# Performance work log

Measured on AMD Instinct MI355X. Metric: run time of the kernel, lower is better.

The kernel has to match this reference:

```python
import jax, jax.numpy as jnp
import numpy as np

N_EXPERTS = 8
EMB = 1024
HID = 2816


def setup_inputs() -> dict:
    key = jax.random.key(0)
    k1, k2, k3, k4, k5 = jax.random.split(key, 5)
    x = jax.random.normal(k1, (2, 2048, EMB), dtype=jnp.float32)
    w_router = jax.random.normal(k2, (EMB, N_EXPERTS), dtype=jnp.float32) * 0.02
    w1 = jax.random.normal(k3, (N_EXPERTS, EMB, HID), dtype=jnp.float32) * 0.02
    w3 = jax.random.normal(k4, (N_EXPERTS, EMB, HID), dtype=jnp.float32) * 0.02
    w2 = jax.random.normal(k5, (N_EXPERTS, HID, EMB), dtype=jnp.float32) * 0.02
    return {"x": x, "w_router": w_router, "w1": w1, "w3": w3, "w2": w2,
            "n_experts_per_token": 2}


def reference(x, w_router, w1, w3, w2, n_experts_per_token):
    # x: (b, s, d) -> flatten to tokens (t, d)
    orig_shape = x.shape
    xf = x.reshape(-1, orig_shape[-1])                      # (t, d)
    scores = xf @ w_router                                  # (t, E)
    top_v, top_i = jax.lax.top_k(scores, n_experts_per_token)  # (t, k)
    top_p = jax.nn.softmax(top_v, axis=-1)                  # (t, k)
    # dense per-token gate over experts (top-k indices are distinct)
    gates = jnp.sum(jax.nn.one_hot(top_i, w_router.shape[-1], dtype=x.dtype)
                    * top_p[..., None], axis=1)             # (t, E)
    # SwiGLU for every expert (dense reference for the masked dispatch)
    h = jnp.einsum('td,edh->teh', xf, w1)                   # (t, E, H)
    g = jnp.einsum('td,edh->teh', xf, w3)                   # (t, E, H)
    expert_out = jnp.einsum('teh,ehd->ted', jax.nn.silu(h) * g, w2)  # (t, E, d)
    y = jnp.einsum('ted,te->td', expert_out, gates)
    return y.reshape(orig_shape)
```

## Files before the change

### kernel.cpp

```cpp
#include <hip/hip_runtime.h>
#include <hip/hip_bf16.h>

#define N_EXPERTS 8
#define EMB 1024
#define HID 2816
#define NTOK 4096
#define NSLOT (NTOK * 2)
#define TLIST NTOK

typedef float f32x4 __attribute__((ext_vector_type(4)));
typedef short short8 __attribute__((ext_vector_type(8)));

static __device__ __forceinline__ unsigned short f2bf(float v) {
    __hip_bfloat16 b = __float2bfloat16(v);
    return *reinterpret_cast<unsigned short*>(&b);
}

static __device__ __forceinline__ void ldst16(const unsigned short* g, unsigned short* l) {
    __builtin_amdgcn_global_load_lds(
        (const __attribute__((address_space(1))) unsigned int*)g,
        (__attribute__((address_space(3))) unsigned int*)l,
        16, 0, 0);
}

__global__ __launch_bounds__(256) void transpose_cvt(const float* __restrict__ in,
                                                     unsigned short* __restrict__ out,
                                                     int R, int C) {
    __shared__ unsigned short tile[64][68];
    int e = blockIdx.z;
    int r0 = blockIdx.y * 64, c0 = blockIdx.x * 64;
    const float* src = in + (size_t)e * R * C;
    unsigned short* dst = out + (size_t)e * R * C;
    int tid = threadIdx.x;
#pragma unroll
    for (int i = 0; i < 4; ++i) {
        int lin = i * 256 + tid;
        int r = lin >> 4, c4 = (lin & 15) * 4;
        float4 v = *(const float4*)&src[(size_t)(r0 + r) * C + c0 + c4];
        ushort4 b;
        b.x = f2bf(v.x); b.y = f2bf(v.y); b.z = f2bf(v.z); b.w = f2bf(v.w);
        *(ushort4*)&tile[r][c4] = b;
    }
    __syncthreads();
#pragma unroll
    for (int i = 0; i < 4; ++i) {
        int lin = i * 256 + tid;
        int c = lin >> 4, r4 = (lin & 15) * 4;
        ushort4 b;
        b.x = tile[r4 + 0][c]; b.y = tile[r4 + 1][c];
        b.z = tile[r4 + 2][c]; b.w = tile[r4 + 3][c];
        *(ushort4*)&dst[(size_t)(c0 + c) * R + r0 + r4] = b;
    }
}

__global__ __launch_bounds__(64) void router_kernel(const float* __restrict__ x,
                                                    const float* __restrict__ wr,
                                                    unsigned short* __restrict__ xbf,
                                                    int* __restrict__ sel,
                                                    float* __restrict__ gates) {
    int t = blockIdx.x, lane = threadIdx.x;
    const float* xr = x + (size_t)t * EMB;
    float acc[N_EXPERTS];
#pragma unroll
    for (int e = 0; e < N_EXPERTS; ++e) acc[e] = 0.f;
    for (int d = lane; d < EMB; d += 64) {
        float xv = xr[d];
        xbf[(size_t)t * EMB + d] = f2bf(xv);
        const float* w = wr + d * N_EXPERTS;
#pragma unroll
        for (int e = 0; e < N_EXPERTS; ++e) acc[e] += xv * w[e];
    }
#pragma unroll
    for (int off = 32; off; off >>= 1) {
#pragma unroll
        for (int e = 0; e < N_EXPERTS; ++e) acc[e] += __shfl_xor(acc[e], off, 64);
    }
    if (lane == 0) {
        int b0 = 0; float v0 = acc[0];
#pragma unroll
        for (int e = 1; e < N_EXPERTS; ++e) if (acc[e] > v0) { v0 = acc[e]; b0 = e; }
        int b1 = -1; float v1 = -1e30f;
#pragma unroll
        for (int e = 0; e < N_EXPERTS; ++e) if (e != b0 && acc[e] > v1) { v1 = acc[e]; b1 = e; }
        float g0 = 1.f / (1.f + expf(v1 - v0));
        float g1 = 1.f - g0;
        sel[t] = b0 | (b1 << 8);
        gates[2 * t] = g0;
        gates[2 * t + 1] = g1;
    }
}

__global__ __launch_bounds__(256) void build_lists(const int* __restrict__ sel,
                                                   int* __restrict__ counts,
                                                   int* __restrict__ lists) {
    int e = blockIdx.x;
    int tid = threadIdx.x, lane = tid & 63, wid = tid >> 6;
    __shared__ int wsum[4];
    __shared__ int running;
    if (tid == 0) running = 0;
    __syncthreads();
    for (int base = 0; base < NTOK; base += 256) {
        int tok = base + tid;
        int s = sel[tok];
        int e0 = s & 0xff, e1 = (s >> 8) & 0xff;
        bool take = (e0 == e) || (e1 == e);
        int slot = (e0 == e) ? 2 * tok : 2 * tok + 1;
        unsigned long long b = __ballot(take);
        int lp = __popcll(b & ((1ull << lane) - 1ull));
        if (lane == 0) wsum[wid] = __popcll(b);
        __syncthreads();
        int off = running;
        for (int w = 0; w < wid; ++w) off += wsum[w];
        if (take) lists[e * TLIST + off + lp] = slot;
        __syncthreads();
        if (tid == 0) running += wsum[0] + wsum[1] + wsum[2] + wsum[3];
        __syncthreads();
    }
    if (tid == 0) counts[e] = running;
}

__global__ __launch_bounds__(256) void gemm1_kernel(const unsigned short* __restrict__ xbf,
                                                    const unsigned short* __restrict__ w1T,
                                                    const unsigned short* __restrict__ w3T,
                                                    unsigned short* __restrict__ h,
                                                    const int* __restrict__ counts,
                                                    const int* __restrict__ lists) {
    int e = blockIdx.z;
    int cnt = counts[e];
    int rt = blockIdx.y;
    if (rt * 128 >= cnt) return;
    int n0 = blockIdx.x * 64;

    __shared__ unsigned short As[128 * 32];
    __shared__ unsigned short B1s[64 * 32];
    __shared__ unsigned short B3s[64 * 32];
    __shared__ int slotArr[128];

    int tid = threadIdx.x;
    if (tid < 128) {
        int r = rt * 128 + tid;
        slotArr[tid] = (r < cnt) ? lists[e * TLIST + r] : -1;
    }
    __syncthreads();

    int lane = tid & 63, wid = tid >> 6;
    int seg = lane >> 2, chunk = lane & 3;

    int rA0 = wid * 32 + seg, rA1 = wid * 32 + 16 + seg;
    int s0 = slotArr[rA0], s1 = slotArr[rA1];
    int t0 = s0 >= 0 ? (s0 >> 1) : 0, t1 = s1 >= 0 ? (s1 >> 1) : 0;
    const unsigned short* gA0 = xbf + (size_t)t0 * EMB + chunk * 8;
    const unsigned short* gA1 = xbf + (size_t)t1 * EMB + chunk * 8;
    int rB = n0 + wid * 16 + seg;
    const unsigned short* gB1 = w1T + ((size_t)e * HID + rB) * EMB + chunk * 8;
    const unsigned short* gB3 = w3T + ((size_t)e * HID + rB) * EMB + chunk * 8;
    unsigned short* lA0 = &As[wid * 1024];
    unsigned short* lA1 = &As[wid * 1024 + 512];
    unsigned short* lB1 = &B1s[wid * 512];
    unsigned short* lB3 = &B3s[wid * 512];

    int wr = wid >> 1, wc = wid & 1;
    int lrow = lane & 15, quad = lane >> 4;

    f32x4 zero4 = {0.f, 0.f, 0.f, 0.f};
    f32x4 acc1[4][2], acc3[4][2];
#pragma unroll
    for (int mt = 0; mt < 4; ++mt)
#pragma unroll
        for (int nt = 0; nt < 2; ++nt) { acc1[mt][nt] = zero4; acc3[mt][nt] = zero4; }

    const int KT = EMB / 32;
    for (int kt = 0; kt < KT; ++kt) {
        ldst16(gA0, lA0); ldst16(gA1, lA1);
        ldst16(gB1, lB1); ldst16(gB3, lB3);
        gA0 += 32; gA1 += 32; gB1 += 32; gB3 += 32;
        __builtin_amdgcn_s_waitcnt(0);
        __syncthreads();
        short8 af[4], b1f[2], b3f[2];
#pragma unroll
        for (int mt = 0; mt < 4; ++mt)
            af[mt] = *(const short8*)&As[(wr * 64 + mt * 16 + lrow) * 32 + quad * 8];
#pragma unroll
        for (int nt = 0; nt < 2; ++nt) {
            b1f[nt] = *(const short8*)&B1s[(wc * 32 + nt * 16 + lrow) * 32 + quad * 8];
            b3f[nt] = *(const short8*)&B3s[(wc * 32 + nt * 16 + lrow) * 32 + quad * 8];
        }
#pragma unroll
        for (int mt = 0; mt < 4; ++mt)
#pragma unroll
            for (int nt = 0; nt < 2; ++nt) {
                acc1[mt][nt] = __builtin_amdgcn_mfma_f32_16x16x32_bf16(af[mt], b1f[nt], acc1[mt][nt], 0, 0, 0);
                acc3[mt][nt] = __builtin_amdgcn_mfma_f32_16x16x32_bf16(af[mt], b3f[nt], acc3[mt][nt], 0, 0, 0);
            }
        __syncthreads();
    }

#pragma unroll
    for (int mt = 0; mt < 4; ++mt) {
#pragma unroll
        for (int i = 0; i < 4; ++i) {
            int r = wr * 64 + mt * 16 + quad * 4 + i;
            int slot = slotArr[r];
            if (slot < 0) continue;
#pragma unroll
            for (int nt = 0; nt < 2; ++nt) {
                float v1 = acc1[mt][nt][i];
                float v3 = acc3[mt][nt][i];
                float hv = v1 / (1.f + __expf(-v1)) * v3;
                int c = n0 + wc * 32 + nt * 16 + lrow;
                h[(size_t)slot * HID + c] = f2bf(hv);
            }
        }
    }
}

__global__ __launch_bounds__(256) void gemm2_kernel(const unsigned short* __restrict__ h,
                                                    const unsigned short* __restrict__ w2T,
                                                    float* __restrict__ oslot,
                                                    const int* __restrict__ counts,
                                                    const int* __restrict__ lists,
                                                    const float* __restrict__ gates) {
    int e = blockIdx.z;
    int cnt = counts[e];
    int rt = blockIdx.y;
    if (rt * 128 >= cnt) return;
    int n0 = blockIdx.x * 128;

    __shared__ unsigned short As[128 * 32];
    __shared__ unsigned short Bs[128 * 32];
    __shared__ int slotArr[128];

    int tid = threadIdx.x;
    if (tid < 128) {
        int r = rt * 128 + tid;
        slotArr[tid] = (r < cnt) ? lists[e * TLIST + r] : -1;
    }
    __syncthreads();

    int lane = tid & 63, wid = tid >> 6;
    int seg = lane >> 2, chunk = lane & 3;

    int rA0 = wid * 32 + seg, rA1 = wid * 32 + 16 + seg;
    int s0 = slotArr[rA0], s1 = slotArr[rA1];
    const unsigned short* gA0 = h + (size_t)(s0 < 0 ? 0 : s0) * HID + chunk * 8;
    const unsigned short* gA1 = h + (size_t)(s1 < 0 ? 0 : s1) * HID + chunk * 8;
    int rB0 = n0 + wid * 32 + seg, rB1 = rB0 + 16;
    const unsigned short* gB0 = w2T + ((size_t)e * EMB + rB0) * HID + chunk * 8;
    const unsigned short* gB1 = w2T + ((size_t)e * EMB + rB1) * HID + chunk * 8;
    unsigned short* lA0 = &As[wid * 1024];
    unsigned short* lA1 = &As[wid * 1024 + 512];
    unsigned short* lB0 = &Bs[wid * 1024];
    unsigned short* lB1 = &Bs[wid * 1024 + 512];

    int wr = wid >> 1, wc = wid & 1;
    int lrow = lane & 15, quad = lane >> 4;

    f32x4 zero4 = {0.f, 0.f, 0.f, 0.f};
    f32x4 acc[4][4];
#pragma unroll
    for (int mt = 0; mt < 4; ++mt)
#pragma unroll
        for (int nt = 0; nt < 4; ++nt) acc[mt][nt] = zero4;

    const int KT = HID / 32;
    for (int kt = 0; kt < KT; ++kt) {
        ldst16(gA0, lA0); ldst16(gA1, lA1);
        ldst16(gB0, lB0); ldst16(gB1, lB1);
        gA0 += 32; gA1 += 32; gB0 += 32; gB1 += 32;
        __builtin_amdgcn_s_waitcnt(0);
        __syncthreads();
        short8 af[4], bf[4];
#pragma unroll
        for (int mt = 0; mt < 4; ++mt)
            af[mt] = *(const short8*)&As[(wr * 64 + mt * 16 + lrow) * 32 + quad * 8];
#pragma unroll
        for (int nt = 0; nt < 4; ++nt)
            bf[nt] = *(const short8*)&Bs[(wc * 64 + nt * 16 + lrow) * 32 + quad * 8];
#pragma unroll
        for (int mt = 0; mt < 4; ++mt)
#pragma unroll
            for (int nt = 0; nt < 4; ++nt)
                acc[mt][nt] = __builtin_amdgcn_mfma_f32_16x16x32_bf16(af[mt], bf[nt], acc[mt][nt], 0, 0, 0);
        __syncthreads();
    }

#pragma unroll
    for (int mt = 0; mt < 4; ++mt) {
#pragma unroll
        for (int i = 0; i < 4; ++i) {
            int r = wr * 64 + mt * 16 + quad * 4 + i;
            int slot = slotArr[r];
            if (slot < 0) continue;
            float g = gates[slot];
#pragma unroll
            for (int nt = 0; nt < 4; ++nt) {
                int c = n0 + wc * 64 + nt * 16 + lrow;
                oslot[(size_t)slot * EMB + c] = g * acc[mt][nt][i];
            }
        }
    }
}

__global__ __launch_bounds__(256) void combine_kernel(const float* __restrict__ oslot,
                                                      float* __restrict__ out) {
    int gid = blockIdx.x * 256 + threadIdx.x;
    int t = gid / (EMB / 4);
    int r = gid % (EMB / 4);
    const float4* a = (const float4*)(oslot + (size_t)(2 * t) * EMB);
    const float4* b = (const float4*)(oslot + (size_t)(2 * t + 1) * EMB);
    float4 va = a[r], vb = b[r];
    float4 vo = {va.x + vb.x, va.y + vb.y, va.z + vb.z, va.w + vb.w};
    ((float4*)out)[gid] = vo;
}

extern "C" void kernel_launch(void* const* d_in, const int* in_sizes, int n_in,
                              void* d_out, int out_size, void* d_ws, size_t ws_size,
                              hipStream_t stream) {
    const float* x = (const float*)d_in[0];
    const float* wrout = (const float*)d_in[1];
    const float* w1 = (const float*)d_in[2];
    const float* w3 = (const float*)d_in[3];
    const float* w2 = (const float*)d_in[4];
    float* out = (float*)d_out;

    char* ws = (char*)d_ws;
    const size_t SW = (size_t)N_EXPERTS * EMB * HID * 2;
    const size_t SX = (size_t)NTOK * EMB * 2;
    const size_t SH = (size_t)NSLOT * HID * 2;
    const size_t SMETA = 256 + (size_t)N_EXPERTS * TLIST * 4 + (size_t)NSLOT * 4 + (size_t)NTOK * 4;
    const size_t NEEDED = 3 * SW + SX + SH + SMETA;
    if (ws_size < NEEDED) return;

    unsigned short* w1T = (unsigned short*)(ws);
    unsigned short* w3T = (unsigned short*)(ws + SW);
    unsigned short* w2T = (unsigned short*)(ws + 2 * SW);
    unsigned short* xbf = (unsigned short*)(ws + 3 * SW);
    unsigned short* hbuf = (unsigned short*)(ws + 3 * SW + SX);
    char* meta = ws + 3 * SW + SX + SH;
    int* counts = (int*)meta;
    int* lists = (int*)(meta + 256);
    float* gates = (float*)(meta + 256 + (size_t)N_EXPERTS * TLIST * 4);
    int* sel = (int*)(meta + 256 + (size_t)N_EXPERTS * TLIST * 4 + (size_t)NSLOT * 4);
    float* oslot = (float*)(ws);

    transpose_cvt<<<dim3(HID / 64, EMB / 64, N_EXPERTS), 256, 0, stream>>>(w1, w1T, EMB, HID);
    transpose_cvt<<<dim3(HID / 64, EMB / 64, N_EXPERTS), 256, 0, stream>>>(w3, w3T, EMB, HID);
    transpose_cvt<<<dim3(EMB / 64, HID / 64, N_EXPERTS), 256, 0, stream>>>(w2, w2T, HID, EMB);

    router_kernel<<<NTOK, 64, 0, stream>>>(x, wrout, xbf, sel, gates);
    build_lists<<<N_EXPERTS, 256, 0, stream>>>(sel, counts, lists);

    gemm1_kernel<<<dim3(HID / 64, NTOK / 128, N_EXPERTS), 256, 0, stream>>>(
        xbf, w1T, w3T, hbuf, counts, lists);
    gemm2_kernel<<<dim3(EMB / 128, NTOK / 128, N_EXPERTS), 256, 0, stream>>>(
        hbuf, w2T, oslot, counts, lists, gates);
    combine_kernel<<<NTOK * EMB / 4 / 256, 256, 0, stream>>>(oslot, out);
}
```

Baseline: 537.2 us.

## Double-buffer expert GEMM tiles, atomically combine outputs, merge weight transposes

Both expert GEMM kernels now use two LDS buffers, issuing the next k-slice's async global-to-LDS loads before computing on the current slice, and drop the explicit full waitcnt. The separate combine pass is removed: gemm2 atomically adds gated results into a pre-zeroed output. The three weight transpose launches are merged into one grid. The aim is to overlap memory latency with MFMA work and cut launches and intermediate traffic. In exchange it adds possible LDS-DMA ordering hazards and nondeterministic fp32 atomic accumulation.

```diff
diff --git a/kernel.cpp b/kernel.cpp
--- a/kernel.cpp
+++ b/kernel.cpp
@@ -23,12 +23,21 @@
         16, 0, 0);
 }
 
-__global__ __launch_bounds__(256) void transpose_cvt(const float* __restrict__ in,
-                                                     unsigned short* __restrict__ out,
-                                                     int R, int C) {
+__global__ __launch_bounds__(256) void transpose_cvt_all(const float* __restrict__ w1,
+                                                         const float* __restrict__ w3,
+                                                         const float* __restrict__ w2,
+                                                         unsigned short* __restrict__ w1T,
+                                                         unsigned short* __restrict__ w3T,
+                                                         unsigned short* __restrict__ w2T) {
     __shared__ unsigned short tile[64][68];
-    int e = blockIdx.z;
-    int r0 = blockIdx.y * 64, c0 = blockIdx.x * 64;
+    int z = blockIdx.z;
+    int which = z >> 3, e = z & 7;
+    const float* in;
+    unsigned short* out;
+    int R, C, r0, c0;
+    if (which == 0)      { in = w1; out = w1T; R = EMB; C = HID; r0 = blockIdx.y * 64; c0 = blockIdx.x * 64; }
+    else if (which == 1) { in = w3; out = w3T; R = EMB; C = HID; r0 = blockIdx.y * 64; c0 = blockIdx.x * 64; }
+    else                 { in = w2; out = w2T; R = HID; C = EMB; r0 = blockIdx.x * 64; c0 = blockIdx.y * 64; }
     const float* src = in + (size_t)e * R * C;
     unsigned short* dst = out + (size_t)e * R * C;
     int tid = threadIdx.x;
@@ -51,6 +60,12 @@
         b.z = tile[r4 + 2][c]; b.w = tile[r4 + 3][c];
         *(ushort4*)&dst[(size_t)(c0 + c) * R + r0 + r4] = b;
     }
+}
+
+__global__ __launch_bounds__(256) void zero_out(float* __restrict__ p) {
+    int gid = blockIdx.x * 256 + threadIdx.x;
+    float4 z = {0.f, 0.f, 0.f, 0.f};
+    ((float4*)p)[gid] = z;
 }
 
 __global__ __launch_bounds__(64) void router_kernel(const float* __restrict__ x,
@@ -131,9 +146,9 @@
     if (rt * 128 >= cnt) return;
     int n0 = blockIdx.x * 64;
 
-    __shared__ unsigned short As[128 * 32];
-    __shared__ unsigned short B1s[64 * 32];
-    __shared__ unsigned short B3s[64 * 32];
+    __shared__ unsigned short As[2][128 * 32];
+    __shared__ unsigned short B1s[2][64 * 32];
+    __shared__ unsigned short B3s[2][64 * 32];
     __shared__ int slotArr[128];
 
     int tid = threadIdx.x;
@@ -154,10 +169,12 @@
     int rB = n0 + wid * 16 + seg;
     const unsigned short* gB1 = w1T + ((size_t)e * HID + rB) * EMB + chunk * 8;
     const unsigned short* gB3 = w3T + ((size_t)e * HID + rB) * EMB + chunk * 8;
-    unsigned short* lA0 = &As[wid * 1024];
-    unsigned short* lA1 = &As[wid * 1024 + 512];
-    unsigned short* lB1 = &B1s[wid * 512];
-    unsigned short* lB3 = &B3s[wid * 512];
+    unsigned short* lA0 = &As[0][wid * 1024];
+    unsigned short* lA1 = &As[0][wid * 1024 + 512];
+    unsigned short* lB1 = &B1s[0][wid * 512];
+    unsigned short* lB3 = &B3s[0][wid * 512];
+    const int DA = 128 * 32;
+    const int DB = 64 * 32;
 
     int wr = wid >> 1, wc = wid & 1;
     int lrow = lane & 15, quad = lane >> 4;
@@ -169,31 +186,45 @@
 #pragma unroll
         for (int nt = 0; nt < 2; ++nt) { acc1[mt][nt] = zero4; acc3[mt][nt] = zero4; }
 
+#define G1_COMPUTE(b) do {                                                                  \
+        short8 af[4], b1f[2], b3f[2];                                                       \
+        _Pragma("unroll")                                                                   \
+        for (int mt = 0; mt < 4; ++mt)                                                      \
+            af[mt] = *(const short8*)&As[b][(wr * 64 + mt * 16 + lrow) * 32 + quad * 8];    \
+        _Pragma("unroll")                                                                   \
+        for (int nt = 0; nt < 2; ++nt) {                                                    \
+            b1f[nt] = *(const short8*)&B1s[b][(wc * 32 + nt * 16 + lrow) * 32 + quad * 8];  \
+            b3f[nt] = *(const short8*)&B3s[b][(wc * 32 + nt * 16 + lrow) * 32 + quad * 8];  \
+        }                                                                                   \
+        _Pragma("unroll")                                                                   \
+        for (int mt = 0; mt < 4; ++mt)                                                      \
+            _Pragma("unroll")                                                               \
+            for (int nt = 0; nt < 2; ++nt) {                                                \
+                acc1[mt][nt] = __builtin_amdgcn_mfma_f32_16x16x32_bf16(af[mt], b1f[nt], acc1[mt][nt], 0, 0, 0); \
+                acc3[mt][nt] = __builtin_amdgcn_mfma_f32_16x16x32_bf16(af[mt], b3f[nt], acc3[mt][nt], 0, 0, 0); \
+            }                                                                               \
+    } while (0)
+
+    ldst16(gA0, lA0); ldst16(gA1, lA1); ldst16(gB1, lB1); ldst16(gB3, lB3);
+    gA0 += 32; gA1 += 32; gB1 += 32; gB3 += 32;
+    __syncthreads();
+
     const int KT = EMB / 32;
-    for (int kt = 0; kt < KT; ++kt) {
-        ldst16(gA0, lA0); ldst16(gA1, lA1);
-        ldst16(gB1, lB1); ldst16(gB3, lB3);
+    for (int kt = 0; kt < KT; kt += 2) {
+        ldst16(gA0, lA0 + DA); ldst16(gA1, lA1 + DA);
+        ldst16(gB1, lB1 + DB); ldst16(gB3, lB3 + DB);
         gA0 += 32; gA1 += 32; gB1 += 32; gB3 += 32;
-        __builtin_amdgcn_s_waitcnt(0);
-        __syncthreads();
-        short8 af[4], b1f[2], b3f[2];
-#pragma unroll
-        for (int mt = 0; mt < 4; ++mt)
-            af[mt] = *(const short8*)&As[(wr * 64 + mt * 16 + lrow) * 32 + quad * 8];
-#pragma unroll
-        for (int nt = 0; nt < 2; ++nt) {
-            b1f[nt] = *(const short8*)&B1s[(wc * 32 + nt * 16 + lrow) * 32 + quad * 8];
-            b3f[nt] = *(const short8*)&B3s[(wc * 32 + nt * 16 + lrow) * 32 + quad * 8];
+        G1_COMPUTE(0);
+        __syncthreads();
+        if (kt + 2 < KT) {
+            ldst16(gA0, lA0); ldst16(gA1, lA1);
+            ldst16(gB1, lB1); ldst16(gB3, lB3);
+            gA0 += 32; gA1 += 32; gB1 += 32; gB3 += 32;
         }
-#pragma unroll
-        for (int mt = 0; mt < 4; ++mt)
-#pragma unroll
-            for (int nt = 0; nt < 2; ++nt) {
-                acc1[mt][nt] = __builtin_amdgcn_mfma_f32_16x16x32_bf16(af[mt], b1f[nt], acc1[mt][nt], 0, 0, 0);
-                acc3[mt][nt] = __builtin_amdgcn_mfma_f32_16x16x32_bf16(af[mt], b3f[nt], acc3[mt][nt], 0, 0, 0);
-            }
-        __syncthreads();
-    }
+        G1_COMPUTE(1);
+        __syncthreads();
+    }
+#undef G1_COMPUTE
 
 #pragma unroll
     for (int mt = 0; mt < 4; ++mt) {
@@ -216,7 +247,7 @@
 
 __global__ __launch_bounds__(256) void gemm2_kernel(const unsigned short* __restrict__ h,
                                                     const unsigned short* __restrict__ w2T,
-                                                    float* __restrict__ oslot,
+                                                    float* __restrict__ out,
                                                     const int* __restrict__ counts,
                                                     const int* __restrict__ lists,
                                                     const float* __restrict__ gates) {
@@ -226,8 +257,8 @@
     if (rt * 128 >= cnt) return;
     int n0 = blockIdx.x * 128;
 
-    __shared__ unsigned short As[128 * 32];
-    __shared__ unsigned short Bs[128 * 32];
+    __shared__ unsigned short As[2][128 * 32];
+    __shared__ unsigned short Bs[2][128 * 32];
     __shared__ int slotArr[128];
 
     int tid = threadIdx.x;
@@ -247,10 +278,11 @@
     int rB0 = n0 + wid * 32 + seg, rB1 = rB0 + 16;
     const unsigned short* gB0 = w2T + ((size_t)e * EMB + rB0) * HID + chunk * 8;
     const unsigned short* gB1 = w2T + ((size_t)e * EMB + rB1) * HID + chunk * 8;
-    unsigned short* lA0 = &As[wid * 1024];
-    unsigned short* lA1 = &As[wid * 1024 + 512];
-    unsigned short* lB0 = &Bs[wid * 1024];
-    unsigned short* lB1 = &Bs[wid * 1024 + 512];
+    unsigned short* lA0 = &As[0][wid * 1024];
+    unsigned short* lA1 = &As[0][wid * 1024 + 512];
+    unsigned short* lB0 = &Bs[0][wid * 1024];
+    unsigned short* lB1 = &Bs[0][wid * 1024 + 512];
+    const int D2 = 128 * 32;
 
     int wr = wid >> 1, wc = wid & 1;
     int lrow = lane & 15, quad = lane >> 4;
@@ -262,27 +294,41 @@
 #pragma unroll
         for (int nt = 0; nt < 4; ++nt) acc[mt][nt] = zero4;
 
+#define G2_COMPUTE(b) do {                                                                  \
+        short8 af[4], bf[4];                                                                \
+        _Pragma("unroll")                                                                   \
+        for (int mt = 0; mt < 4; ++mt)                                                      \
+            af[mt] = *(const short8*)&As[b][(wr * 64 + mt * 16 + lrow) * 32 + quad * 8];    \
+        _Pragma("unroll")                                                                   \
+        for (int nt = 0; nt < 4; ++nt)                                                      \
+            bf[nt] = *(const short8*)&Bs[b][(wc * 64 + nt * 16 + lrow) * 32 + quad * 8];    \
+        _Pragma("unroll")                                                                   \
+        for (int mt = 0; mt < 4; ++mt)                                                      \
+            _Pragma("unroll")                                                               \
+            for (int nt = 0; nt < 4; ++nt)                                                  \
+                acc[mt][nt] = __builtin_amdgcn_mfma_f32_16x16x32_bf16(af[mt], bf[nt], acc[mt][nt], 0, 0, 0); \
+    } while (0)
+
+    ldst16(gA0, lA0); ldst16(gA1, lA1); ldst16(gB0, lB0); ldst16(gB1, lB1);
+    gA0 += 32; gA1 += 32; gB0 += 32; gB1 += 32;
+    __syncthreads();
+
     const int KT = HID / 32;
-    for (int kt = 0; kt < KT; ++kt) {
-        ldst16(gA0, lA0); ldst16(gA1, lA1);
-        ldst16(gB0, lB0); ldst16(gB1, lB1);
+    for (int kt = 0; kt < KT; kt += 2) {
+        ldst16(gA0, lA0 + D2); ldst16(gA1, lA1 + D2);
+        ldst16(gB0, lB0 + D2); ldst16(gB1, lB1 + D2);
         gA0 += 32; gA1 += 32; gB0 += 32; gB1 += 32;
-        __builtin_amdgcn_s_waitcnt(0);
-        __syncthreads();
-        short8 af[4], bf[4];
-#pragma unroll
-        for (int mt = 0; mt < 4; ++mt)
-            af[mt] = *(const short8*)&As[(wr * 64 + mt * 16 + lrow) * 32 + quad * 8];
-#pragma unroll
-        for (int nt = 0; nt < 4; ++nt)
-            bf[nt] = *(const short8*)&Bs[(wc * 64 + nt * 16 + lrow) * 32 + quad * 8];
-#pragma unroll
-        for (int mt = 0; mt < 4; ++mt)
-#pragma unroll
-            for (int nt = 0; nt < 4; ++nt)
-                acc[mt][nt] = __builtin_amdgcn_mfma_f32_16x16x32_bf16(af[mt], bf[nt], acc[mt][nt], 0, 0, 0);
-        __syncthreads();
-    }
+        G2_COMPUTE(0);
+        __syncthreads();
+        if (kt + 2 < KT) {
+            ldst16(gA0, lA0); ldst16(gA1, lA1);
+            ldst16(gB0, lB0); ldst16(gB1, lB1);
+            gA0 += 32; gA1 += 32; gB0 += 32; gB1 += 32;
+        }
+        G2_COMPUTE(1);
+        __syncthreads();
+    }
+#undef G2_COMPUTE
 
 #pragma unroll
     for (int mt = 0; mt < 4; ++mt) {
@@ -292,25 +338,14 @@
             int slot = slotArr[r];
             if (slot < 0) continue;
             float g = gates[slot];
+            int tok = slot >> 1;
 #pragma unroll
             for (int nt = 0; nt < 4; ++nt) {
                 int c = n0 + wc * 64 + nt * 16 + lrow;
-                oslot[(size_t)slot * EMB + c] = g * acc[mt][nt][i];
+                atomicAdd(&out[(size_t)tok * EMB + c], g * acc[mt][nt][i]);
             }
         }
     }
-}
-
-__global__ __launch_bounds__(256) void combine_kernel(const float* __restrict__ oslot,
-                                                      float* __restrict__ out) {
-    int gid = blockIdx.x * 256 + threadIdx.x;
-    int t = gid / (EMB / 4);
-    int r = gid % (EMB / 4);
-    const float4* a = (const float4*)(oslot + (size_t)(2 * t) * EMB);
-    const float4* b = (const float4*)(oslot + (size_t)(2 * t + 1) * EMB);
-    float4 va = a[r], vb = b[r];
-    float4 vo = {va.x + vb.x, va.y + vb.y, va.z + vb.z, va.w + vb.w};
-    ((float4*)out)[gid] = vo;
 }
 
 extern "C" void kernel_launch(void* const* d_in, const int* in_sizes, int n_in,
@@ -341,11 +376,11 @@
     int* lists = (int*)(meta + 256);
     float* gates = (float*)(meta + 256 + (size_t)N_EXPERTS * TLIST * 4);
     int* sel = (int*)(meta + 256 + (size_t)N_EXPERTS * TLIST * 4 + (size_t)NSLOT * 4);
-    float* oslot = (float*)(ws);
-
-    transpose_cvt<<<dim3(HID / 64, EMB / 64, N_EXPERTS), 256, 0, stream>>>(w1, w1T, EMB, HID);
-    transpose_cvt<<<dim3(HID / 64, EMB / 64, N_EXPERTS), 256, 0, stream>>>(w3, w3T, EMB, HID);
-    transpose_cvt<<<dim3(EMB / 64, HID / 64, N_EXPERTS), 256, 0, stream>>>(w2, w2T, HID, EMB);
+
+    transpose_cvt_all<<<dim3(HID / 64, EMB / 64, 3 * N_EXPERTS), 256, 0, stream>>>(
+        w1, w3, w2, w1T, w3T, w2T);
+
+    zero_out<<<NTOK * EMB / 4 / 256, 256, 0, stream>>>(out);
 
     router_kernel<<<NTOK, 64, 0, stream>>>(x, wrout, xbf, sel, gates);
     build_lists<<<N_EXPERTS, 256, 0, stream>>>(sel, counts, lists);
@@ -353,6 +388,5 @@
     gemm1_kernel<<<dim3(HID / 64, NTOK / 128, N_EXPERTS), 256, 0, stream>>>(
         xbf, w1T, w3T, hbuf, counts, lists);
     gemm2_kernel<<<dim3(EMB / 128, NTOK / 128, N_EXPERTS), 256, 0, stream>>>(
-        hbuf, w2T, oslot, counts, lists, gates);
-    combine_kernel<<<NTOK * EMB / 4 / 256, 256, 0, stream>>>(oslot, out);
-}
+        hbuf, w2T, out, counts, lists, gates);
+}
```

Result: slower. 648.5 us (+20.7%).
